# Kernel tuning notes

Hardware: AMD Instinct MI355X
Metric: run time of the kernel (lower is better)

The kernel has to match this reference:

```python
import jax, jax.numpy as jnp
import numpy as np

B, T, Z, S, H = 32, 128, 100, 6, 64
F1, F2 = 512, 128


def setup_inputs() -> dict:
    key = jax.random.key(0)
    ks = jax.random.split(key, 11)
    g = lambda k, shape, sc: (jax.random.normal(k, shape, dtype=jnp.float32) * sc)
    return {
        "x": jax.random.normal(ks[0], (B, T, Z, S), dtype=jnp.float32),
        "W_ih": g(ks[1], (3 * H, S), 0.125),   # GRU input weights [r|z|n]
        "W_hh": g(ks[2], (3 * H, H), 0.125),   # GRU hidden weights [r|z|n]
        "b_ih": g(ks[3], (3 * H,), 0.125),
        "b_hh": g(ks[4], (3 * H,), 0.125),
        "w1": g(ks[5], (F1, H), 0.1),
        "b1": g(ks[6], (F1,), 0.1),
        "w2": g(ks[7], (F2, F1), 0.04),
        "b2": g(ks[8], (F2,), 0.04),
        "w3": g(ks[9], (1, F2), 0.09),
        "b3": g(ks[10], (1,), 0.09),
    }


def reference(x, W_ih, W_hh, b_ih, b_hh, w1, b1, w2, b2, w3, b3):
    b, t, z, s = x.shape
    h_dim = W_hh.shape[1]
    # Fuse the per-zone python loop into the batch dim, zone-major so the
    # final reshape matches torch.stack(a).view(-1, t, nzones).
    xm = jnp.transpose(x, (2, 0, 1, 3)).reshape(z * b, t, s)  # (ZB, T, S)
    # Precompute input projections for all timesteps (one big GEMM).
    gi_all = jnp.einsum('nts,gs->ntg', xm, W_ih) + b_ih        # (ZB, T, 3H)

    def step(h, gi):
        gh = h @ W_hh.T + b_hh
        r = jax.nn.sigmoid(gi[:, :h_dim] + gh[:, :h_dim])
        zg = jax.nn.sigmoid(gi[:, h_dim:2 * h_dim] + gh[:, h_dim:2 * h_dim])
        n = jnp.tanh(gi[:, 2 * h_dim:] + r * gh[:, 2 * h_dim:])
        h_new = (1.0 - zg) * n + zg * h
        return h_new, h_new

    h0 = jnp.zeros((z * b, h_dim), x.dtype)
    _, sx = jax.lax.scan(step, h0, jnp.swapaxes(gi_all, 0, 1))  # (T, ZB, H)
    sx = jnp.swapaxes(sx, 0, 1)                                  # (ZB, T, H)

    a1 = jax.nn.relu(sx @ w1.T + b1)
    a2 = jax.nn.relu(a1 @ w2.T + b2)
    a3 = a2 @ w3.T + b3                                          # (ZB, T, 1)
    return a3.reshape(-1, t, z)                                  # (B, T, Z)
```

## Files before the change

### kernel.cpp

```cpp
#include <hip/hip_runtime.h>
#include <stdint.h>

#define Tdim 128
#define Zdim 100
#define Sdim 6
#define Hdim 64
#define ZB   3200
#define F1   512
#define F2   128
#define Mrows (ZB * Tdim)

typedef _Float16 f16x8 __attribute__((ext_vector_type(8)));
typedef _Float16 f16x4 __attribute__((ext_vector_type(4)));
typedef float f32x4 __attribute__((ext_vector_type(4)));
typedef uint32_t u32x4 __attribute__((ext_vector_type(4)));

__device__ __forceinline__ float fast_rcp(float x) {
  return __builtin_amdgcn_rcpf(x);
}

__global__ __launch_bounds__(256) void prep_kernel(
    const float* __restrict__ W_ih, const float* __restrict__ W_hh,
    const float* __restrict__ w1, const float* __restrict__ w2,
    _Float16* __restrict__ Wf, _Float16* __restrict__ w1p,
    _Float16* __restrict__ w2p) {
  int i = blockIdx.x * 256 + threadIdx.x;
  if (i < 192 * 96) {
    int g = i / 96, k = i - g * 96;
    float v = (k < 64) ? W_hh[g * 64 + k] : ((k < 70) ? W_ih[g * 6 + (k - 64)] : 0.f);
    Wf[i] = (_Float16)v;
  }
  int j = i - 192 * 96;
  if (j >= 0 && j < 32768) {
    int kt = j >> 11, ntl = (j >> 10) & 1, kf = (j >> 9) & 1;
    int lane = (j >> 3) & 63, e = j & 7;
    int q = lane >> 4, c = lane & 15;
    int row = kt * 32 + ntl * 16 + c;
    int h = kf * 32 + q * 8 + e;
    w1p[j] = (_Float16)w1[row * 64 + h];
  }
  int l = j - 32768;
  if (l >= 0 && l < 65536) {
    int kt = l >> 12, nt = (l >> 9) & 7;
    int lane = (l >> 3) & 63, e = l & 7;
    int q = lane >> 4, c = lane & 15;
    int row = nt * 16 + c;
    int k = kt * 32 + q * 8 + e;
    w2p[l] = (_Float16)w2[row * 512 + k];
  }
}

__global__ __launch_bounds__(256, 2) void gru_kernel(
    const float* __restrict__ x, const _Float16* __restrict__ Wf,
    const float* __restrict__ b_ih, const float* __restrict__ b_hh,
    _Float16* __restrict__ sx) {
  __shared__ __align__(16) _Float16 hist[16][32][72];
  __shared__ __align__(16) _Float16 xs[Tdim][32][8];
  const int tid = threadIdx.x;
  const int lane = tid & 63;
  const int w = tid >> 6;
  const int c = lane & 15;
  const int q = lane >> 4;

  for (int i = 0; i < 16; i++) {
    int idx = i * 256 + tid;
    int t = idx >> 5, row = idx & 31;
    int nr = blockIdx.x * 32 + row;
    const float* p = x + (size_t)(nr & 31) * (Tdim * Zdim * Sdim)
                       + (size_t)t * (Zdim * Sdim) + (size_t)(nr >> 5) * Sdim;
    f16x8 v;
    v[0] = (_Float16)p[0]; v[1] = (_Float16)p[1]; v[2] = (_Float16)p[2];
    v[3] = (_Float16)p[3]; v[4] = (_Float16)p[4]; v[5] = (_Float16)p[5];
    v[6] = (_Float16)0.f;  v[7] = (_Float16)0.f;
    *(f16x8*)&xs[t][row][0] = v;
  }

  const int gr0 = w * 16;
  const int gz0 = 64 + w * 16;
  const int gn0 = 128 + w * 16;

  f16x8 Ar[3], Az[3], Anh[2], Ani;
#pragma unroll
  for (int kf = 0; kf < 3; kf++) {
    Ar[kf] = *(const f16x8*)(Wf + (size_t)(gr0 + c) * 96 + kf * 32 + q * 8);
    Az[kf] = *(const f16x8*)(Wf + (size_t)(gz0 + c) * 96 + kf * 32 + q * 8);
  }
  Anh[0] = *(const f16x8*)(Wf + (size_t)(gn0 + c) * 96 + q * 8);
  Anh[1] = *(const f16x8*)(Wf + (size_t)(gn0 + c) * 96 + 32 + q * 8);
  Ani    = *(const f16x8*)(Wf + (size_t)(gn0 + c) * 96 + 64 + q * 8);

  f32x4 Cr, Cz, Cnh, Cni;
  {
    f32x4 bir = *(const f32x4*)(b_ih + gr0 + q * 4);
    f32x4 bhr = *(const f32x4*)(b_hh + gr0 + q * 4);
    f32x4 biz = *(const f32x4*)(b_ih + gz0 + q * 4);
    f32x4 bhz = *(const f32x4*)(b_hh + gz0 + q * 4);
#pragma unroll
    for (int r = 0; r < 4; r++) { Cr[r] = bir[r] + bhr[r]; Cz[r] = biz[r] + bhz[r]; }
    Cnh = *(const f32x4*)(b_hh + gn0 + q * 4);
    Cni = *(const f32x4*)(b_ih + gn0 + q * 4);
  }

  const uint32_t xmask = (q == 0) ? 0xffffffffu : 0u;

  __syncthreads();

  f16x8 Bh0[2], Bh1[2];
  f32x4 hprev[2];
#pragma unroll
  for (int cg = 0; cg < 2; cg++) {
    Bh0[cg] = (f16x8){0, 0, 0, 0, 0, 0, 0, 0};
    Bh1[cg] = (f16x8){0, 0, 0, 0, 0, 0, 0, 0};
    hprev[cg] = (f32x4){0.f, 0.f, 0.f, 0.f};
  }

  f32x4 Sr[2], Sz[2], Sni[2];
#pragma unroll
  for (int cg = 0; cg < 2; cg++) {
    u32x4 xv = *(const u32x4*)&xs[0][cg * 16 + c][0];
    xv[0] &= xmask; xv[1] &= xmask; xv[2] &= xmask; xv[3] &= xmask;
    f16x8 Bx = *(f16x8*)&xv;
    Sni[cg] = __builtin_amdgcn_mfma_f32_16x16x32_f16(Ani, Bx, Cni, 0, 0, 0);
    Sr[cg]  = __builtin_amdgcn_mfma_f32_16x16x32_f16(Ar[2], Bx, Cr, 0, 0, 0);
    Sz[cg]  = __builtin_amdgcn_mfma_f32_16x16x32_f16(Az[2], Bx, Cz, 0, 0, 0);
  }

#pragma unroll 1
  for (int tch = 0; tch < 8; tch++) {
#pragma unroll 1
    for (int tc = 0; tc < 16; tc++) {
      const int t = tch * 16 + tc;
      f32x4 Dnh[2], Dr[2], Dz[2];
#pragma unroll
      for (int cg = 0; cg < 2; cg++)
        Dnh[cg] = __builtin_amdgcn_mfma_f32_16x16x32_f16(Anh[0], Bh0[cg], Cnh, 0, 0, 0);
#pragma unroll
      for (int cg = 0; cg < 2; cg++)
        Dr[cg] = __builtin_amdgcn_mfma_f32_16x16x32_f16(Ar[0], Bh0[cg], Sr[cg], 0, 0, 0);
#pragma unroll
      for (int cg = 0; cg < 2; cg++)
        Dz[cg] = __builtin_amdgcn_mfma_f32_16x16x32_f16(Az[0], Bh0[cg], Sz[cg], 0, 0, 0);
#pragma unroll
      for (int cg = 0; cg < 2; cg++)
        Dnh[cg] = __builtin_amdgcn_mfma_f32_16x16x32_f16(Anh[1], Bh1[cg], Dnh[cg], 0, 0, 0);
#pragma unroll
      for (int cg = 0; cg < 2; cg++)
        Dr[cg] = __builtin_amdgcn_mfma_f32_16x16x32_f16(Ar[1], Bh1[cg], Dr[cg], 0, 0, 0);
#pragma unroll
      for (int cg = 0; cg < 2; cg++)
        Dz[cg] = __builtin_amdgcn_mfma_f32_16x16x32_f16(Az[1], Bh1[cg], Dz[cg], 0, 0, 0);

#pragma unroll
      for (int cg = 0; cg < 2; cg++) {
        f16x4 pk;
#pragma unroll
        for (int r = 0; r < 4; r++) {
          float er = __expf(-Dr[cg][r]);
          float rr = fast_rcp(1.f + er);
          float ez = __expf(-Dz[cg][r]);
          float zg = fast_rcp(1.f + ez);
          float na = Sni[cg][r] + rr * Dnh[cg][r];
          float en = __expf(2.f * na);
          float nn = 1.f - 2.f * fast_rcp(en + 1.f);
          float hnew = nn + zg * (hprev[cg][r] - nn);
          hprev[cg][r] = hnew;
          pk[r] = (_Float16)hnew;
        }
        *(f16x4*)&hist[tc][cg * 16 + c][w * 16 + q * 4] = pk;
      }

      if (t + 1 < Tdim) {
#pragma unroll
        for (int cg = 0; cg < 2; cg++) {
          u32x4 xv = *(const u32x4*)&xs[t + 1][cg * 16 + c][0];
          xv[0] &= xmask; xv[1] &= xmask; xv[2] &= xmask; xv[3] &= xmask;
          f16x8 Bx = *(f16x8*)&xv;
          Sni[cg] = __builtin_amdgcn_mfma_f32_16x16x32_f16(Ani, Bx, Cni, 0, 0, 0);
          Sr[cg]  = __builtin_amdgcn_mfma_f32_16x16x32_f16(Ar[2], Bx, Cr, 0, 0, 0);
          Sz[cg]  = __builtin_amdgcn_mfma_f32_16x16x32_f16(Az[2], Bx, Cz, 0, 0, 0);
        }
      }
      __syncthreads();
#pragma unroll
      for (int cg = 0; cg < 2; cg++) {
        Bh0[cg] = *(const f16x8*)&hist[tc][cg * 16 + c][q * 8];
        Bh1[cg] = *(const f16x8*)&hist[tc][cg * 16 + c][32 + q * 8];
      }
    }
    {
      const int t0 = tch * 16;
#pragma unroll
      for (int rr2 = 0; rr2 < 8; rr2++) {
        const int row = w * 8 + rr2;
        const int nrow = blockIdx.x * 32 + row;
        _Float16* dst = sx + (size_t)nrow * Tdim * Hdim + (size_t)t0 * Hdim;
#pragma unroll
        for (int it = 0; it < 2; it++) {
          int idx = it * 64 + lane;
          int tcc = idx >> 3, hd8 = idx & 7;
          f16x8 vv = *(const f16x8*)&hist[tcc][row][hd8 * 8];
          *(f16x8*)(dst + tcc * 64 + hd8 * 8) = vv;
        }
      }
      __syncthreads();
    }
  }
}

__global__ __launch_bounds__(256, 2) void mlp_kernel(
    const _Float16* __restrict__ sx, const _Float16* __restrict__ w1p,
    const _Float16* __restrict__ w2p, const float* __restrict__ b1,
    const float* __restrict__ b2, const float* __restrict__ w3,
    const float* __restrict__ b3, float* __restrict__ out) {
  __shared__ __align__(16) _Float16 w1s[32768];
  __shared__ __align__(16) _Float16 rep[4][4][512];
  const int tid = threadIdx.x;
  const int lane = tid & 63;
  const int wave = tid >> 6;
  const int c = lane & 15;
  const int q = lane >> 4;
  const size_t m0 = ((size_t)blockIdx.x * 4 + wave) * 64;

  {
    const u32x4* src = (const u32x4*)w1p;
    u32x4* dst = (u32x4*)w1s;
#pragma unroll
    for (int i = 0; i < 16; i++)
      dst[i * 256 + tid] = src[i * 256 + tid];
  }

  f16x8 Bs[4][2];
#pragma unroll
  for (int g = 0; g < 4; g++)
#pragma unroll
    for (int kk = 0; kk < 2; kk++)
      Bs[g][kk] = *(const f16x8*)(sx + (m0 + g * 16 + c) * Hdim + kk * 32 + q * 8);

  f32x4 acc2[4][8];
#pragma unroll
  for (int g = 0; g < 4; g++)
#pragma unroll
    for (int nt = 0; nt < 8; nt++) acc2[g][nt] = (f32x4){0.f, 0.f, 0.f, 0.f};

  __syncthreads();

  {
#pragma unroll
    for (int ntl = 0; ntl < 2; ntl++) {
      f16x8 A0 = *(const f16x8*)&w1s[ntl * 1024 + lane * 8];
      f16x8 A1 = *(const f16x8*)&w1s[ntl * 1024 + 512 + lane * 8];
      f32x4 bb = *(const f32x4*)(b1 + ntl * 16 + q * 4);
      const int roff = ((2 * ntl + (q >> 1)) * 16 + c) * 8 + (q & 1) * 4;
#pragma unroll
      for (int g = 0; g < 4; g++) {
        f32x4 cc = __builtin_amdgcn_mfma_f32_16x16x32_f16(A0, Bs[g][0], bb, 0, 0, 0);
        cc = __builtin_amdgcn_mfma_f32_16x16x32_f16(A1, Bs[g][1], cc, 0, 0, 0);
        f16x4 pk;
#pragma unroll
        for (int r = 0; r < 4; r++)
          pk[r] = (_Float16)(cc[r] > 0.f ? cc[r] : 0.f);
        *(f16x4*)&rep[wave][g][roff] = pk;
      }
    }
  }

#pragma unroll 1
  for (int kt = 0; kt < 16; kt++) {
    const int ktn = kt + 1;
    const bool more = (ktn < 16);
    f16x8 A2[8];
#pragma unroll
    for (int nt = 0; nt < 8; nt++)
      A2[nt] = *(const f16x8*)(w2p + (size_t)kt * 4096 + nt * 512 + lane * 8);
    f16x8 W0[2], W1[2];
    f32x4 bb[2];
    {
      const int kts = more ? ktn : kt;
#pragma unroll
      for (int ntl = 0; ntl < 2; ntl++) {
        W0[ntl] = *(const f16x8*)&w1s[kts * 2048 + ntl * 1024 + lane * 8];
        W1[ntl] = *(const f16x8*)&w1s[kts * 2048 + ntl * 1024 + 512 + lane * 8];
        bb[ntl] = *(const f32x4*)(b1 + kts * 32 + ntl * 16 + q * 4);
      }
    }
    f16x8 Ba[4];
#pragma unroll
    for (int g = 0; g < 4; g++)
      Ba[g] = *(const f16x8*)&rep[wave][g][lane * 8];

    if (more) {
#pragma unroll
      for (int ntl = 0; ntl < 2; ntl++) {
        const int roff = ((2 * ntl + (q >> 1)) * 16 + c) * 8 + (q & 1) * 4;
#pragma unroll
        for (int g = 0; g < 4; g++) {
          f32x4 cc = __builtin_amdgcn_mfma_f32_16x16x32_f16(W0[ntl], Bs[g][0], bb[ntl], 0, 0, 0);
          cc = __builtin_amdgcn_mfma_f32_16x16x32_f16(W1[ntl], Bs[g][1], cc, 0, 0, 0);
          f16x4 pk;
#pragma unroll
          for (int r = 0; r < 4; r++)
            pk[r] = (_Float16)(cc[r] > 0.f ? cc[r] : 0.f);
          *(f16x4*)&rep[wave][g][roff] = pk;
        }
      }
    }

#pragma unroll
    for (int nt = 0; nt < 8; nt++)
#pragma unroll
      for (int g = 0; g < 4; g++)
        acc2[g][nt] = __builtin_amdgcn_mfma_f32_16x16x32_f16(A2[nt], Ba[g], acc2[g][nt], 0, 0, 0);
  }

  float part[4] = {0.f, 0.f, 0.f, 0.f};
#pragma unroll
  for (int nt = 0; nt < 8; nt++) {
    f32x4 bb = *(const f32x4*)(b2 + nt * 16 + q * 4);
    f32x4 ww = *(const f32x4*)(w3 + nt * 16 + q * 4);
#pragma unroll
    for (int g = 0; g < 4; g++) {
#pragma unroll
      for (int r = 0; r < 4; r++) {
        float v = acc2[g][nt][r] + bb[r];
        v = v > 0.f ? v : 0.f;
        part[g] = fmaf(v, ww[r], part[g]);
      }
    }
  }
#pragma unroll
  for (int g = 0; g < 4; g++) {
    part[g] += __shfl_xor(part[g], 16, 64);
    part[g] += __shfl_xor(part[g], 32, 64);
  }
  float pv = (q == 0) ? part[0] : (q == 1) ? part[1] : (q == 2) ? part[2] : part[3];
  out[m0 + q * 16 + c] = pv + b3[0];
}

extern "C" void kernel_launch(void* const* d_in, const int* in_sizes, int n_in,
                              void* d_out, int out_size, void* d_ws, size_t ws_size,
                              hipStream_t stream) {
  const float* x    = (const float*)d_in[0];
  const float* W_ih = (const float*)d_in[1];
  const float* W_hh = (const float*)d_in[2];
  const float* b_ih = (const float*)d_in[3];
  const float* b_hh = (const float*)d_in[4];
  const float* w1   = (const float*)d_in[5];
  const float* b1   = (const float*)d_in[6];
  const float* w2   = (const float*)d_in[7];
  const float* b2   = (const float*)d_in[8];
  const float* w3   = (const float*)d_in[9];
  const float* b3   = (const float*)d_in[10];
  float* out = (float*)d_out;

  char* ws = (char*)d_ws;
  _Float16* sxf = (_Float16*)ws;
  _Float16* Wf  = (_Float16*)(ws + 52428800);
  _Float16* w1p = (_Float16*)(ws + 52428800 + 36864);
  _Float16* w2p = (_Float16*)(ws + 52428800 + 36864 + 65536);

  hipLaunchKernelGGL(prep_kernel, dim3(456), dim3(256), 0, stream,
                     W_ih, W_hh, w1, w2, Wf, w1p, w2p);
  hipLaunchKernelGGL(gru_kernel, dim3(ZB / 32), dim3(256), 0, stream,
                     x, Wf, b_ih, b_hh, sxf);
  hipLaunchKernelGGL(mlp_kernel, dim3(Mrows / 256), dim3(256), 0, stream,
                     sxf, w1p, w2p, b1, b2, w3, b3, out);
}
```

Before: 257.6 us.

## Fuse GRU and MLP into one persistent kernel with flag-based streaming handoff

Merges the GRU and MLP kernels into one launch. An atomic ticket hands out roles, so the 100 GRU blocks start first, and the MLP blocks spin on per-(sequence block, time chunk) flags so the MLP on a 16-step chunk overlaps with the GRU recurrence still running. The GRU also drops its shared-memory x staging and loads each step's x straight from global one step ahead, and the MLP tiling is remapped to (sequence, time-chunk) tiles. The spin-waits depend on GRU blocks being resident ahead of MLP blocks, and MLP blocks holding CUs while they wait could reduce throughput.

```diff
diff --git a/kernel.cpp b/kernel.cpp
--- a/kernel.cpp
+++ b/kernel.cpp
@@ -9,10 +9,13 @@
 #define F1   512
 #define F2   128
 #define Mrows (ZB * Tdim)
+#define NGRU 100
+#define NMLP 1600
 
 typedef _Float16 f16x8 __attribute__((ext_vector_type(8)));
 typedef _Float16 f16x4 __attribute__((ext_vector_type(4)));
 typedef float f32x4 __attribute__((ext_vector_type(4)));
+typedef float f32x2 __attribute__((ext_vector_type(2)));
 typedef uint32_t u32x4 __attribute__((ext_vector_type(4)));
 
 __device__ __forceinline__ float fast_rcp(float x) {
@@ -23,8 +26,9 @@
     const float* __restrict__ W_ih, const float* __restrict__ W_hh,
     const float* __restrict__ w1, const float* __restrict__ w2,
     _Float16* __restrict__ Wf, _Float16* __restrict__ w1p,
-    _Float16* __restrict__ w2p) {
+    _Float16* __restrict__ w2p, unsigned int* __restrict__ sync) {
   int i = blockIdx.x * 256 + threadIdx.x;
+  if (i < 801) sync[i] = 0u;
   if (i < 192 * 96) {
     int g = i / 96, k = i - g * 96;
     float v = (k < 64) ? W_hh[g * 64 + k] : ((k < 70) ? W_ih[g * 6 + (k - 64)] : 0.f);
@@ -50,290 +54,334 @@
   }
 }
 
-__global__ __launch_bounds__(256, 2) void gru_kernel(
+__global__ __launch_bounds__(256, 2) void fused_kernel(
     const float* __restrict__ x, const _Float16* __restrict__ Wf,
     const float* __restrict__ b_ih, const float* __restrict__ b_hh,
-    _Float16* __restrict__ sx) {
-  __shared__ __align__(16) _Float16 hist[16][32][72];
-  __shared__ __align__(16) _Float16 xs[Tdim][32][8];
+    _Float16* __restrict__ sx, const _Float16* __restrict__ w1p,
+    const _Float16* __restrict__ w2p, const float* __restrict__ b1,
+    const float* __restrict__ b2, const float* __restrict__ w3,
+    const float* __restrict__ b3, float* __restrict__ out,
+    unsigned int* __restrict__ flags, unsigned int* __restrict__ ticket) {
+  union SmemU {
+    unsigned int tk;
+    struct { _Float16 hist[16][32][72]; } g;
+    struct { _Float16 w1s[32768]; _Float16 rep[4][4][512]; } m;
+  };
+  __shared__ __align__(16) SmemU smem;
   const int tid = threadIdx.x;
+  if (tid == 0) smem.tk = atomicAdd(ticket, 1u);
+  __syncthreads();
+  const int tk = (int)smem.tk;
+  __syncthreads();
+
   const int lane = tid & 63;
   const int w = tid >> 6;
   const int c = lane & 15;
   const int q = lane >> 4;
 
-  for (int i = 0; i < 16; i++) {
-    int idx = i * 256 + tid;
-    int t = idx >> 5, row = idx & 31;
-    int nr = blockIdx.x * 32 + row;
-    const float* p = x + (size_t)(nr & 31) * (Tdim * Zdim * Sdim)
-                       + (size_t)t * (Zdim * Sdim) + (size_t)(nr >> 5) * Sdim;
-    f16x8 v;
-    v[0] = (_Float16)p[0]; v[1] = (_Float16)p[1]; v[2] = (_Float16)p[2];
-    v[3] = (_Float16)p[3]; v[4] = (_Float16)p[4]; v[5] = (_Float16)p[5];
-    v[6] = (_Float16)0.f;  v[7] = (_Float16)0.f;
-    *(f16x8*)&xs[t][row][0] = v;
-  }
-
-  const int gr0 = w * 16;
-  const int gz0 = 64 + w * 16;
-  const int gn0 = 128 + w * 16;
-
-  f16x8 Ar[3], Az[3], Anh[2], Ani;
-#pragma unroll
-  for (int kf = 0; kf < 3; kf++) {
-    Ar[kf] = *(const f16x8*)(Wf + (size_t)(gr0 + c) * 96 + kf * 32 + q * 8);
-    Az[kf] = *(const f16x8*)(Wf + (size_t)(gz0 + c) * 96 + kf * 32 + q * 8);
-  }
-  Anh[0] = *(const f16x8*)(Wf + (size_t)(gn0 + c) * 96 + q * 8);
-  Anh[1] = *(const f16x8*)(Wf + (size_t)(gn0 + c) * 96 + 32 + q * 8);
-  Ani    = *(const f16x8*)(Wf + (size_t)(gn0 + c) * 96 + 64 + q * 8);
-
-  f32x4 Cr, Cz, Cnh, Cni;
-  {
-    f32x4 bir = *(const f32x4*)(b_ih + gr0 + q * 4);
-    f32x4 bhr = *(const f32x4*)(b_hh + gr0 + q * 4);
-    f32x4 biz = *(const f32x4*)(b_ih + gz0 + q * 4);
-    f32x4 bhz = *(const f32x4*)(b_hh + gz0 + q * 4);
-#pragma unroll
-    for (int r = 0; r < 4; r++) { Cr[r] = bir[r] + bhr[r]; Cz[r] = biz[r] + bhz[r]; }
-    Cnh = *(const f32x4*)(b_hh + gn0 + q * 4);
-    Cni = *(const f32x4*)(b_ih + gn0 + q * 4);
-  }
-
-  const uint32_t xmask = (q == 0) ? 0xffffffffu : 0u;
-
-  __syncthreads();
-
-  f16x8 Bh0[2], Bh1[2];
-  f32x4 hprev[2];
-#pragma unroll
-  for (int cg = 0; cg < 2; cg++) {
-    Bh0[cg] = (f16x8){0, 0, 0, 0, 0, 0, 0, 0};
-    Bh1[cg] = (f16x8){0, 0, 0, 0, 0, 0, 0, 0};
-    hprev[cg] = (f32x4){0.f, 0.f, 0.f, 0.f};
-  }
-
-  f32x4 Sr[2], Sz[2], Sni[2];
-#pragma unroll
-  for (int cg = 0; cg < 2; cg++) {
-    u32x4 xv = *(const u32x4*)&xs[0][cg * 16 + c][0];
-    xv[0] &= xmask; xv[1] &= xmask; xv[2] &= xmask; xv[3] &= xmask;
-    f16x8 Bx = *(f16x8*)&xv;
-    Sni[cg] = __builtin_amdgcn_mfma_f32_16x16x32_f16(Ani, Bx, Cni, 0, 0, 0);
-    Sr[cg]  = __builtin_amdgcn_mfma_f32_16x16x32_f16(Ar[2], Bx, Cr, 0, 0, 0);
-    Sz[cg]  = __builtin_amdgcn_mfma_f32_16x16x32_f16(Az[2], Bx, Cz, 0, 0, 0);
-  }
+  if (tk < NGRU) {
+    const int gb = tk;
+    auto& hist = smem.g.hist;
+
+    const float* px[2];
+#pragma unroll
+    for (int cg = 0; cg < 2; cg++) {
+      int nr = gb * 32 + cg * 16 + c;
+      px[cg] = x + (size_t)(nr & 31) * (Tdim * Zdim * Sdim)
+                 + (size_t)(nr >> 5) * Sdim;
+    }
+
+    const int gr0 = w * 16;
+    const int gz0 = 64 + w * 16;
+    const int gn0 = 128 + w * 16;
+
+    f16x8 Ar[3], Az[3], Anh[2], Ani;
+#pragma unroll
+    for (int kf = 0; kf < 3; kf++) {
+      Ar[kf] = *(const f16x8*)(Wf + (size_t)(gr0 + c) * 96 + kf * 32 + q * 8);
+      Az[kf] = *(const f16x8*)(Wf + (size_t)(gz0 + c) * 96 + kf * 32 + q * 8);
+    }
+    Anh[0] = *(const f16x8*)(Wf + (size_t)(gn0 + c) * 96 + q * 8);
+    Anh[1] = *(const f16x8*)(Wf + (size_t)(gn0 + c) * 96 + 32 + q * 8);
+    Ani    = *(const f16x8*)(Wf + (size_t)(gn0 + c) * 96 + 64 + q * 8);
+
+    f32x4 Cr, Cz, Cnh, Cni;
+    {
+      f32x4 bir = *(const f32x4*)(b_ih + gr0 + q * 4);
+      f32x4 bhr = *(const f32x4*)(b_hh + gr0 + q * 4);
+      f32x4 biz = *(const f32x4*)(b_ih + gz0 + q * 4);
+      f32x4 bhz = *(const f32x4*)(b_hh + gz0 + q * 4);
+#pragma unroll
+      for (int r = 0; r < 4; r++) { Cr[r] = bir[r] + bhr[r]; Cz[r] = biz[r] + bhz[r]; }
+      Cnh = *(const f32x4*)(b_hh + gn0 + q * 4);
+      Cni = *(const f32x4*)(b_ih + gn0 + q * 4);
+    }
+
+    const uint32_t xmask = (q == 0) ? 0xffffffffu : 0u;
+
+    f16x8 Bh0[2], Bh1[2];
+    f32x4 hprev[2];
+#pragma unroll
+    for (int cg = 0; cg < 2; cg++) {
+      Bh0[cg] = (f16x8){0, 0, 0, 0, 0, 0, 0, 0};
+      Bh1[cg] = (f16x8){0, 0, 0, 0, 0, 0, 0, 0};
+      hprev[cg] = (f32x4){0.f, 0.f, 0.f, 0.f};
+    }
+
+    f32x2 xa[2], xb[2], xc[2];
+    f32x4 Sr[2], Sz[2], Sni[2];
+#pragma unroll
+    for (int cg = 0; cg < 2; cg++) {
+      xa[cg] = *(const f32x2*)(px[cg] + 0);
+      xb[cg] = *(const f32x2*)(px[cg] + 2);
+      xc[cg] = *(const f32x2*)(px[cg] + 4);
+    }
+#pragma unroll
+    for (int cg = 0; cg < 2; cg++) {
+      f16x8 Bx;
+      Bx[0] = (_Float16)xa[cg][0]; Bx[1] = (_Float16)xa[cg][1];
+      Bx[2] = (_Float16)xb[cg][0]; Bx[3] = (_Float16)xb[cg][1];
+      Bx[4] = (_Float16)xc[cg][0]; Bx[5] = (_Float16)xc[cg][1];
+      Bx[6] = (_Float16)0.f;       Bx[7] = (_Float16)0.f;
+      u32x4 xv = *(u32x4*)&Bx;
+      xv[0] &= xmask; xv[1] &= xmask; xv[2] &= xmask; xv[3] &= xmask;
+      Bx = *(f16x8*)&xv;
+      Sni[cg] = __builtin_amdgcn_mfma_f32_16x16x32_f16(Ani, Bx, Cni, 0, 0, 0);
+      Sr[cg]  = __builtin_amdgcn_mfma_f32_16x16x32_f16(Ar[2], Bx, Cr, 0, 0, 0);
+      Sz[cg]  = __builtin_amdgcn_mfma_f32_16x16x32_f16(Az[2], Bx, Cz, 0, 0, 0);
+    }
 
 #pragma unroll 1
-  for (int tch = 0; tch < 8; tch++) {
+    for (int tch = 0; tch < 8; tch++) {
 #pragma unroll 1
-    for (int tc = 0; tc < 16; tc++) {
-      const int t = tch * 16 + tc;
-      f32x4 Dnh[2], Dr[2], Dz[2];
-#pragma unroll
-      for (int cg = 0; cg < 2; cg++)
-        Dnh[cg] = __builtin_amdgcn_mfma_f32_16x16x32_f16(Anh[0], Bh0[cg], Cnh, 0, 0, 0);
-#pragma unroll
-      for (int cg = 0; cg < 2; cg++)
-        Dr[cg] = __builtin_amdgcn_mfma_f32_16x16x32_f16(Ar[0], Bh0[cg], Sr[cg], 0, 0, 0);
-#pragma unroll
-      for (int cg = 0; cg < 2; cg++)
-        Dz[cg] = __builtin_amdgcn_mfma_f32_16x16x32_f16(Az[0], Bh0[cg], Sz[cg], 0, 0, 0);
-#pragma unroll
-      for (int cg = 0; cg < 2; cg++)
-        Dnh[cg] = __builtin_amdgcn_mfma_f32_16x16x32_f16(Anh[1], Bh1[cg], Dnh[cg], 0, 0, 0);
-#pragma unroll
-      for (int cg = 0; cg < 2; cg++)
-        Dr[cg] = __builtin_amdgcn_mfma_f32_16x16x32_f16(Ar[1], Bh1[cg], Dr[cg], 0, 0, 0);
-#pragma unroll
-      for (int cg = 0; cg < 2; cg++)
-        Dz[cg] = __builtin_amdgcn_mfma_f32_16x16x32_f16(Az[1], Bh1[cg], Dz[cg], 0, 0, 0);
-
-#pragma unroll
-      for (int cg = 0; cg < 2; cg++) {
-        f16x4 pk;
-#pragma unroll
-        for (int r = 0; r < 4; r++) {
-          float er = __expf(-Dr[cg][r]);
-          float rr = fast_rcp(1.f + er);
-          float ez = __expf(-Dz[cg][r]);
-          float zg = fast_rcp(1.f + ez);
-          float na = Sni[cg][r] + rr * Dnh[cg][r];
-          float en = __expf(2.f * na);
-          float nn = 1.f - 2.f * fast_rcp(en + 1.f);
-          float hnew = nn + zg * (hprev[cg][r] - nn);
-          hprev[cg][r] = hnew;
-          pk[r] = (_Float16)hnew;
-        }
-        *(f16x4*)&hist[tc][cg * 16 + c][w * 16 + q * 4] = pk;
-      }
-
-      if (t + 1 < Tdim) {
+      for (int tc = 0; tc < 16; tc++) {
+        const int t = tch * 16 + tc;
+        const int tn = (t + 1 < Tdim) ? t + 1 : Tdim - 1;
 #pragma unroll
         for (int cg = 0; cg < 2; cg++) {
-          u32x4 xv = *(const u32x4*)&xs[t + 1][cg * 16 + c][0];
-          xv[0] &= xmask; xv[1] &= xmask; xv[2] &= xmask; xv[3] &= xmask;
-          f16x8 Bx = *(f16x8*)&xv;
-          Sni[cg] = __builtin_amdgcn_mfma_f32_16x16x32_f16(Ani, Bx, Cni, 0, 0, 0);
-          Sr[cg]  = __builtin_amdgcn_mfma_f32_16x16x32_f16(Ar[2], Bx, Cr, 0, 0, 0);
-          Sz[cg]  = __builtin_amdgcn_mfma_f32_16x16x32_f16(Az[2], Bx, Cz, 0, 0, 0);
-        }
-      }
-      __syncthreads();
-#pragma unroll
-      for (int cg = 0; cg < 2; cg++) {
-        Bh0[cg] = *(const f16x8*)&hist[tc][cg * 16 + c][q * 8];
-        Bh1[cg] = *(const f16x8*)&hist[tc][cg * 16 + c][32 + q * 8];
-      }
-    }
+          const float* pn = px[cg] + (size_t)tn * (Zdim * Sdim);
+          xa[cg] = *(const f32x2*)(pn + 0);
+          xb[cg] = *(const f32x2*)(pn + 2);
+          xc[cg] = *(const f32x2*)(pn + 4);
+        }
+
+        f32x4 Dnh[2], Dr[2], Dz[2];
+#pragma unroll
+        for (int cg = 0; cg < 2; cg++)
+          Dnh[cg] = __builtin_amdgcn_mfma_f32_16x16x32_f16(Anh[0], Bh0[cg], Cnh, 0, 0, 0);
+#pragma unroll
+        for (int cg = 0; cg < 2; cg++)
+          Dr[cg] = __builtin_amdgcn_mfma_f32_16x16x32_f16(Ar[0], Bh0[cg], Sr[cg], 0, 0, 0);
+#pragma unroll
+        for (int cg = 0; cg < 2; cg++)
+          Dz[cg] = __builtin_amdgcn_mfma_f32_16x16x32_f16(Az[0], Bh0[cg], Sz[cg], 0, 0, 0);
+#pragma unroll
+        for (int cg = 0; cg < 2; cg++)
+          Dnh[cg] = __builtin_amdgcn_mfma_f32_16x16x32_f16(Anh[1], Bh1[cg], Dnh[cg], 0, 0, 0);
+#pragma unroll
+        for (int cg = 0; cg < 2; cg++)
+          Dr[cg] = __builtin_amdgcn_mfma_f32_16x16x32_f16(Ar[1], Bh1[cg], Dr[cg], 0, 0, 0);
+#pragma unroll
+        for (int cg = 0; cg < 2; cg++)
+          Dz[cg] = __builtin_amdgcn_mfma_f32_16x16x32_f16(Az[1], Bh1[cg], Dz[cg], 0, 0, 0);
+
+#pragma unroll
+        for (int cg = 0; cg < 2; cg++) {
+          f16x4 pk;
+#pragma unroll
+          for (int r = 0; r < 4; r++) {
+            float er = __expf(-Dr[cg][r]);
+            float rr = fast_rcp(1.f + er);
+            float ez = __expf(-Dz[cg][r]);
+            float zg = fast_rcp(1.f + ez);
+            float na = Sni[cg][r] + rr * Dnh[cg][r];
+            float en = __expf(2.f * na);
+            float nn = 1.f - 2.f * fast_rcp(en + 1.f);
+            float hnew = nn + zg * (hprev[cg][r] - nn);
+            hprev[cg][r] = hnew;
+            pk[r] = (_Float16)hnew;
+          }
+          *(f16x4*)&hist[tc][cg * 16 + c][w * 16 + q * 4] = pk;
+        }
+
+        if (t + 1 < Tdim) {
+#pragma unroll
+          for (int cg = 0; cg < 2; cg++) {
+            f16x8 Bx;
+            Bx[0] = (_Float16)xa[cg][0]; Bx[1] = (_Float16)xa[cg][1];
+            Bx[2] = (_Float16)xb[cg][0]; Bx[3] = (_Float16)xb[cg][1];
+            Bx[4] = (_Float16)xc[cg][0]; Bx[5] = (_Float16)xc[cg][1];
+            Bx[6] = (_Float16)0.f;       Bx[7] = (_Float16)0.f;
+            u32x4 xv = *(u32x4*)&Bx;
+            xv[0] &= xmask; xv[1] &= xmask; xv[2] &= xmask; xv[3] &= xmask;
+            Bx = *(f16x8*)&xv;
+            Sni[cg] = __builtin_amdgcn_mfma_f32_16x16x32_f16(Ani, Bx, Cni, 0, 0, 0);
+            Sr[cg]  = __builtin_amdgcn_mfma_f32_16x16x32_f16(Ar[2], Bx, Cr, 0, 0, 0);
+            Sz[cg]  = __builtin_amdgcn_mfma_f32_16x16x32_f16(Az[2], Bx, Cz, 0, 0, 0);
+          }
+        }
+        __syncthreads();
+#pragma unroll
+        for (int cg = 0; cg < 2; cg++) {
+          Bh0[cg] = *(const f16x8*)&hist[tc][cg * 16 + c][q * 8];
+          Bh1[cg] = *(const f16x8*)&hist[tc][cg * 16 + c][32 + q * 8];
+        }
+      }
+      {
+        const int t0 = tch * 16;
+#pragma unroll
+        for (int rr2 = 0; rr2 < 8; rr2++) {
+          const int row = w * 8 + rr2;
+          const int nrow = gb * 32 + row;
+          _Float16* dst = sx + (size_t)nrow * Tdim * Hdim + (size_t)t0 * Hdim;
+#pragma unroll
+          for (int it = 0; it < 2; it++) {
+            int idx = it * 64 + lane;
+            int tcc = idx >> 3, hd8 = idx & 7;
+            f16x8 vv = *(const f16x8*)&hist[tcc][row][hd8 * 8];
+            *(f16x8*)(dst + tcc * 64 + hd8 * 8) = vv;
+          }
+        }
+        __syncthreads();
+        if (tid == 0) {
+          __threadfence();
+          atomicAdd(&flags[gb * 8 + tch], 1u);
+        }
+      }
+    }
+  } else {
+    const int mid = tk - NGRU;
+    const int ch  = mid / 200;
+    const int rem = mid - ch * 200;
+    const int gbm = rem % NGRU;
+    const int half = rem / NGRU;
+    auto& w1s = smem.m.w1s;
+    auto& rep = smem.m.rep;
+
     {
-      const int t0 = tch * 16;
-#pragma unroll
-      for (int rr2 = 0; rr2 < 8; rr2++) {
-        const int row = w * 8 + rr2;
-        const int nrow = blockIdx.x * 32 + row;
-        _Float16* dst = sx + (size_t)nrow * Tdim * Hdim + (size_t)t0 * Hdim;
-#pragma unroll
-        for (int it = 0; it < 2; it++) {
-          int idx = it * 64 + lane;
-          int tcc = idx >> 3, hd8 = idx & 7;
-          f16x8 vv = *(const f16x8*)&hist[tcc][row][hd8 * 8];
-          *(f16x8*)(dst + tcc * 64 + hd8 * 8) = vv;
-        }
-      }
-      __syncthreads();
-    }
-  }
-}
-
-__global__ __launch_bounds__(256, 2) void mlp_kernel(
-    const _Float16* __restrict__ sx, const _Float16* __restrict__ w1p,
-    const _Float16* __restrict__ w2p, const float* __restrict__ b1,
-    const float* __restrict__ b2, const float* __restrict__ w3,
-    const float* __restrict__ b3, float* __restrict__ out) {
-  __shared__ __align__(16) _Float16 w1s[32768];
-  __shared__ __align__(16) _Float16 rep[4][4][512];
-  const int tid = threadIdx.x;
-  const int lane = tid & 63;
-  const int wave = tid >> 6;
-  const int c = lane & 15;
-  const int q = lane >> 4;
-  const size_t m0 = ((size_t)blockIdx.x * 4 + wave) * 64;
-
-  {
-    const u32x4* src = (const u32x4*)w1p;
-    u32x4* dst = (u32x4*)w1s;
-#pragma unroll
-    for (int i = 0; i < 16; i++)
-      dst[i * 256 + tid] = src[i * 256 + tid];
-  }
-
-  f16x8 Bs[4][2];
-#pragma unroll
-  for (int g = 0; g < 4; g++)
-#pragma unroll
-    for (int kk = 0; kk < 2; kk++)
-      Bs[g][kk] = *(const f16x8*)(sx + (m0 + g * 16 + c) * Hdim + kk * 32 + q * 8);
-
-  f32x4 acc2[4][8];
-#pragma unroll
-  for (int g = 0; g < 4; g++)
-#pragma unroll
-    for (int nt = 0; nt < 8; nt++) acc2[g][nt] = (f32x4){0.f, 0.f, 0.f, 0.f};
-
-  __syncthreads();
-
-  {
-#pragma unroll
-    for (int ntl = 0; ntl < 2; ntl++) {
-      f16x8 A0 = *(const f16x8*)&w1s[ntl * 1024 + lane * 8];
-      f16x8 A1 = *(const f16x8*)&w1s[ntl * 1024 + 512 + lane * 8];
-      f32x4 bb = *(const f32x4*)(b1 + ntl * 16 + q * 4);
-      const int roff = ((2 * ntl + (q >> 1)) * 16 + c) * 8 + (q & 1) * 4;
-#pragma unroll
-      for (int g = 0; g < 4; g++) {
-        f32x4 cc = __builtin_amdgcn_mfma_f32_16x16x32_f16(A0, Bs[g][0], bb, 0, 0, 0);
-        cc = __builtin_amdgcn_mfma_f32_16x16x32_f16(A1, Bs[g][1], cc, 0, 0, 0);
-        f16x4 pk;
-#pragma unroll
-        for (int r = 0; r < 4; r++)
-          pk[r] = (_Float16)(cc[r] > 0.f ? cc[r] : 0.f);
-        *(f16x4*)&rep[wave][g][roff] = pk;
-      }
-    }
-  }
-
-#pragma unroll 1
-  for (int kt = 0; kt < 16; kt++) {
-    const int ktn = kt + 1;
-    const bool more = (ktn < 16);
-    f16x8 A2[8];
-#pragma unroll
-    for (int nt = 0; nt < 8; nt++)
-      A2[nt] = *(const f16x8*)(w2p + (size_t)kt * 4096 + nt * 512 + lane * 8);
-    f16x8 W0[2], W1[2];
-    f32x4 bb[2];
+      const u32x4* srcw = (const u32x4*)w1p;
+      u32x4* dstw = (u32x4*)w1s;
+#pragma unroll
+      for (int i = 0; i < 16; i++)
+        dstw[i * 256 + tid] = srcw[i * 256 + tid];
+    }
+    if (tid == 0) {
+      while (__hip_atomic_load(&flags[gbm * 8 + ch], __ATOMIC_RELAXED,
+                               __HIP_MEMORY_SCOPE_AGENT) == 0u)
+        __builtin_amdgcn_s_sleep(2);
+      (void)__hip_atomic_load(&flags[gbm * 8 + ch], __ATOMIC_ACQUIRE,
+                              __HIP_MEMORY_SCOPE_AGENT);
+    }
+    __syncthreads();
+
+    const int seqB = gbm * 32 + half * 16 + w * 4;
+    const size_t tB = (size_t)ch * 16;
+
+    f16x8 Bs[4][2];
+#pragma unroll
+    for (int g = 0; g < 4; g++)
+#pragma unroll
+      for (int kk = 0; kk < 2; kk++)
+        Bs[g][kk] = *(const f16x8*)(sx + ((size_t)(seqB + g) * Tdim + tB + c) * Hdim
+                                    + kk * 32 + q * 8);
+
+    f32x4 acc2[4][8];
+#pragma unroll
+    for (int g = 0; g < 4; g++)
+#pragma unroll
+      for (int nt = 0; nt < 8; nt++) acc2[g][nt] = (f32x4){0.f, 0.f, 0.f, 0.f};
+
     {
-      const int kts = more ? ktn : kt;
 #pragma unroll
       for (int ntl = 0; ntl < 2; ntl++) {
-        W0[ntl] = *(const f16x8*)&w1s[kts * 2048 + ntl * 1024 + lane * 8];
-        W1[ntl] = *(const f16x8*)&w1s[kts * 2048 + ntl * 1024 + 512 + lane * 8];
-        bb[ntl] = *(const f32x4*)(b1 + kts * 32 + ntl * 16 + q * 4);
-      }
-    }
-    f16x8 Ba[4];
-#pragma unroll
-    for (int g = 0; g < 4; g++)
-      Ba[g] = *(const f16x8*)&rep[wave][g][lane * 8];
-
-    if (more) {
-#pragma unroll
-      for (int ntl = 0; ntl < 2; ntl++) {
+        f16x8 A0 = *(const f16x8*)&w1s[ntl * 1024 + lane * 8];
+        f16x8 A1 = *(const f16x8*)&w1s[ntl * 1024 + 512 + lane * 8];
+        f32x4 bb = *(const f32x4*)(b1 + ntl * 16 + q * 4);
         const int roff = ((2 * ntl + (q >> 1)) * 16 + c) * 8 + (q & 1) * 4;
 #pragma unroll
         for (int g = 0; g < 4; g++) {
-          f32x4 cc = __builtin_amdgcn_mfma_f32_16x16x32_f16(W0[ntl], Bs[g][0], bb[ntl], 0, 0, 0);
-          cc = __builtin_amdgcn_mfma_f32_16x16x32_f16(W1[ntl], Bs[g][1], cc, 0, 0, 0);
+          f32x4 cc = __builtin_amdgcn_mfma_f32_16x16x32_f16(A0, Bs[g][0], bb, 0, 0, 0);
+          cc = __builtin_amdgcn_mfma_f32_16x16x32_f16(A1, Bs[g][1], cc, 0, 0, 0);
           f16x4 pk;
 #pragma unroll
           for (int r = 0; r < 4; r++)
             pk[r] = (_Float16)(cc[r] > 0.f ? cc[r] : 0.f);
-          *(f16x4*)&rep[wave][g][roff] = pk;
-        }
-      }
-    }
-
-#pragma unroll
-    for (int nt = 0; nt < 8; nt++)
+          *(f16x4*)&rep[w][g][roff] = pk;
+        }
+      }
+    }
+
+#pragma unroll 1
+    for (int kt = 0; kt < 16; kt++) {
+      const int ktn = kt + 1;
+      const bool more = (ktn < 16);
+      f16x8 A2[8];
+#pragma unroll
+      for (int nt = 0; nt < 8; nt++)
+        A2[nt] = *(const f16x8*)(w2p + (size_t)kt * 4096 + nt * 512 + lane * 8);
+      f16x8 W0[2], W1[2];
+      f32x4 bb[2];
+      {
+        const int kts = more ? ktn : kt;
+#pragma unroll
+        for (int ntl = 0; ntl < 2; ntl++) {
+          W0[ntl] = *(const f16x8*)&w1s[kts * 2048 + ntl * 1024 + lane * 8];
+          W1[ntl] = *(const f16x8*)&w1s[kts * 2048 + ntl * 1024 + 512 + lane * 8];
+          bb[ntl] = *(const f32x4*)(b1 + kts * 32 + ntl * 16 + q * 4);
+        }
+      }
+      f16x8 Ba[4];
 #pragma unroll
       for (int g = 0; g < 4; g++)
-        acc2[g][nt] = __builtin_amdgcn_mfma_f32_16x16x32_f16(A2[nt], Ba[g], acc2[g][nt], 0, 0, 0);
+        Ba[g] = *(const f16x8*)&rep[w][g][lane * 8];
+
+      if (more) {
+#pragma unroll
+        for (int ntl = 0; ntl < 2; ntl++) {
+          const int roff = ((2 * ntl + (q >> 1)) * 16 + c) * 8 + (q & 1) * 4;
+#pragma unroll
+          for (int g = 0; g < 4; g++) {
+            f32x4 cc = __builtin_amdgcn_mfma_f32_16x16x32_f16(W0[ntl], Bs[g][0], bb[ntl], 0, 0, 0);
+            cc = __builtin_amdgcn_mfma_f32_16x16x32_f16(W1[ntl], Bs[g][1], cc, 0, 0, 0);
+            f16x4 pk;
+#pragma unroll
+            for (int r = 0; r < 4; r++)
+              pk[r] = (_Float16)(cc[r] > 0.f ? cc[r] : 0.f);
+            *(f16x4*)&rep[w][g][roff] = pk;
+          }
+        }
+      }
+
+#pragma unroll
+      for (int nt = 0; nt < 8; nt++)
+#pragma unroll
+        for (int g = 0; g < 4; g++)
+          acc2[g][nt] = __builtin_amdgcn_mfma_f32_16x16x32_f16(A2[nt], Ba[g], acc2[g][nt], 0, 0, 0);
+    }
+
+    float part[4] = {0.f, 0.f, 0.f, 0.f};
+#pragma unroll
+    for (int nt = 0; nt < 8; nt++) {
+      f32x4 bb = *(const f32x4*)(b2 + nt * 16 + q * 4);
+      f32x4 ww = *(const f32x4*)(w3 + nt * 16 + q * 4);
+#pragma unroll
+      for (int g = 0; g < 4; g++) {
+#pragma unroll
+        for (int r = 0; r < 4; r++) {
+          float v = acc2[g][nt][r] + bb[r];
+          v = v > 0.f ? v : 0.f;
+          part[g] = fmaf(v, ww[r], part[g]);
+        }
+      }
+    }
+#pragma unroll
+    for (int g = 0; g < 4; g++) {
+      part[g] += __shfl_xor(part[g], 16, 64);
+      part[g] += __shfl_xor(part[g], 32, 64);
+    }
+    float pv = (q == 0) ? part[0] : (q == 1) ? part[1] : (q == 2) ? part[2] : part[3];
+    out[(size_t)(seqB + q) * Tdim + tB + c] = pv + b3[0];
   }
-
-  float part[4] = {0.f, 0.f, 0.f, 0.f};
-#pragma unroll
-  for (int nt = 0; nt < 8; nt++) {
-    f32x4 bb = *(const f32x4*)(b2 + nt * 16 + q * 4);
-    f32x4 ww = *(const f32x4*)(w3 + nt * 16 + q * 4);
-#pragma unroll
-    for (int g = 0; g < 4; g++) {
-#pragma unroll
-      for (int r = 0; r < 4; r++) {
-        float v = acc2[g][nt][r] + bb[r];
-        v = v > 0.f ? v : 0.f;
-        part[g] = fmaf(v, ww[r], part[g]);
-      }
-    }
-  }
-#pragma unroll
-  for (int g = 0; g < 4; g++) {
-    part[g] += __shfl_xor(part[g], 16, 64);
-    part[g] += __shfl_xor(part[g], 32, 64);
-  }
-  float pv = (q == 0) ? part[0] : (q == 1) ? part[1] : (q == 2) ? part[2] : part[3];
-  out[m0 + q * 16 + c] = pv + b3[0];
 }
 
 extern "C" void kernel_launch(void* const* d_in, const int* in_sizes, int n_in,
@@ -357,11 +405,13 @@
   _Float16* Wf  = (_Float16*)(ws + 52428800);
   _Float16* w1p = (_Float16*)(ws + 52428800 + 36864);
   _Float16* w2p = (_Float16*)(ws + 52428800 + 36864 + 65536);
+  unsigned int* syncb = (unsigned int*)(ws + 52428800 + 36864 + 65536 + 131072);
+  unsigned int* flags  = syncb;
+  unsigned int* ticket = syncb + 800;
 
   hipLaunchKernelGGL(prep_kernel, dim3(456), dim3(256), 0, stream,
-                     W_ih, W_hh, w1, w2, Wf, w1p, w2p);
-  hipLaunchKernelGGL(gru_kernel, dim3(ZB / 32), dim3(256), 0, stream,
-                     x, Wf, b_ih, b_hh, sxf);
-  hipLaunchKernelGGL(mlp_kernel, dim3(Mrows / 256), dim3(256), 0, stream,
-                     sxf, w1p, w2p, b1, b2, w3, b3, out);
+                     W_ih, W_hh, w1, w2, Wf, w1p, w2p, syncb);
+  hipLaunchKernelGGL(fused_kernel, dim3(NGRU + NMLP), dim3(256), 0, stream,
+                     x, Wf, b_ih, b_hh, sxf, w1p, w2p, b1, b2, w3, b3, out,
+                     flags, ticket);
 }
```

Measured after the change: 297.7 us. 15.6% more time.
